# Kernel optimization log

Hardware: AMD Instinct MI355X
Metric: run time of the kernel (lower is better)

## Reference

```python
import jax, jax.numpy as jnp
import numpy as np

BS, NN = 4096, 16          # batch size, robots per sample
OBS_PN, ACT_PN = 10, 2     # per-node obs / action dims
HID = 128                  # hidden_dim; hidden_depth = 2
N = BS * NN                # total nodes


def _build_edges():
    # complete graph per sample including self-loops (PyG GCNConv adds self-loops;
    # self-loop weight exp(-0)=1 matches PyG fill_value=1.0)
    s = np.repeat(np.arange(NN), NN)
    d = np.tile(np.arange(NN), NN)
    off = np.repeat(np.arange(BS) * NN, NN * NN)
    src = np.tile(s, BS) + off
    dst = np.tile(d, BS) + off
    return jnp.asarray(src, jnp.int32), jnp.asarray(dst, jnp.int32)


def setup_inputs() -> dict:
    key = jax.random.key(0)
    ks = jax.random.split(key, 16)
    inp = {
        "obs": jax.random.normal(ks[0], (BS, NN * OBS_PN), jnp.float32),
        "action": jax.random.normal(ks[1], (BS, NN * ACT_PN), jnp.float32),
    }
    dims = [(OBS_PN, HID), (HID, HID), (HID, 1)]  # trunk_input_size = 10
    i = 2
    for q in ("Q1", "Q2"):
        for l, (din, dout) in enumerate(dims):
            inp[f"{q}_W{l}"] = jax.random.normal(ks[i], (din, dout), jnp.float32) / np.sqrt(din).astype(np.float32)
            inp[f"{q}_b{l}"] = jnp.zeros((dout,), jnp.float32)
            i += 1
    inp["src"], inp["dst"] = _build_edges()
    return inp


def _gcn(x, W, b, src, dst, norm):
    # GCNConv: out = scatter_add(norm * (x @ W)[src] -> dst) + b
    y = x @ W                                  # [N, F_out]
    msg = norm[:, None] * y[src]               # [E, F_out]
    return jax.ops.segment_sum(msg, dst, num_segments=N) + b


def reference(obs, action, Q1_W0, Q1_b0, Q1_W1, Q1_b1, Q1_W2, Q1_b2,
              Q2_W0, Q2_b0, Q2_W1, Q2_b1, Q2_W2, Q2_b2, src, dst):
    feat = jnp.concatenate(
        [obs.reshape(N, OBS_PN), action.reshape(N, ACT_PN)], axis=-1)  # [N, 12]
    loc = feat[:, :2]          # robot_loc
    x = feat[:, ACT_PN:]       # input_features[:, gnn_action_dim:] -> [N, 10]

    # per-edge distance weights + symmetric GCN normalization
    w = jnp.exp(-jnp.linalg.norm(loc[dst] - loc[src], axis=-1))        # [E]
    deg = jax.ops.segment_sum(w, dst, num_segments=N)                  # [N]
    dinv = jnp.where(deg > 0, deg, 1.0) ** -0.5
    norm = dinv[src] * w * dinv[dst]

    def net(W0, b0, W1, b1, W2, b2):
        h = jax.nn.relu(_gcn(x, W0, b0, src, dst, norm))
        h = jax.nn.relu(_gcn(h, W1, b1, src, dst, norm))
        return _gcn(h, W2, b2, src, dst, norm).reshape(BS, NN)

    q1 = net(Q1_W0, Q1_b0, Q1_W1, Q1_b1, Q1_W2, Q1_b2)
    q2 = net(Q2_W0, Q2_b0, Q2_W1, Q2_b1, Q2_W2, Q2_b2)
    return (q1, q2)
```

## Files before the change

### kernel.cpp

```cpp
#include <hip/hip_runtime.h>


typedef short    s16x8 __attribute__((ext_vector_type(8)));
typedef float    f32x4 __attribute__((ext_vector_type(4)));
typedef unsigned u32x4 __attribute__((ext_vector_type(4)));

#define MFMA32(a, b, c) __builtin_amdgcn_mfma_f32_16x16x32_bf16((a), (b), (c), 0, 0, 0)

constexpr int WS_W0F = 0;
constexpr int WS_W1  = 8192;

constexpr int LDS_RAW    = 65536;
constexpr int SMEM_TOTAL = 65536 + 8 * 200 * 4;

__device__ __forceinline__ unsigned short bf16_rn(float f) {
  unsigned u = __float_as_uint(f);
  u = u + 0x7FFFu + ((u >> 16) & 1u);
  return (unsigned short)(u >> 16);
}
__device__ __forceinline__ void split2(float f, unsigned short& h, unsigned short& l) {
  h = bf16_rn(f);
  float fh = __uint_as_float(((unsigned)h) << 16);
  l = bf16_rn(f - fh);
}
__device__ __forceinline__ void split_pk(float f0, float f1,
                                         unsigned& H, unsigned& L) {
  unsigned u0 = __float_as_uint(f0) + 0x8000u;
  unsigned u1 = __float_as_uint(f1) + 0x8000u;
  H = __builtin_amdgcn_perm(u1, u0, 0x07060302u);
  float r0 = f0 - __uint_as_float(u0 & 0xFFFF0000u);
  float r1 = f1 - __uint_as_float(u1 & 0xFFFF0000u);
  L = __builtin_amdgcn_perm(__float_as_uint(r1), __float_as_uint(r0), 0x07060302u);
}
__device__ __forceinline__ s16x8 as_s16x8(u32x4 v) {
  return __builtin_bit_cast(s16x8, v);
}

extern "C" __global__ void __launch_bounds__(256)
prep_weights(const float* __restrict__ w0a, const float* __restrict__ w1a,
             const float* __restrict__ w0b, const float* __restrict__ w1b,
             unsigned short* __restrict__ ws) {
  const int tid = threadIdx.x;
  if (blockIdx.x < 16) {
    int f = blockIdx.x * 256 + tid;
    int lane = f & 63, t = (f >> 6) & 7, q = (f >> 9) & 3, net = f >> 11;
    const float* W1 = net ? w1b : w1a;
    int c = 16 * t + (lane & 15);
    int kbase = 32 * q + 4 * (lane >> 4);
    s16x8 v;
#pragma unroll
    for (int e = 0; e < 8; ++e) {
      int k = kbase + (e & 3) + 16 * (e >> 2);
      v[e] = (short)bf16_rn(W1[k * 128 + c]);
    }
    ((s16x8*)(ws + WS_W1))[((net * 4 + q) * 8 + t) * 64 + lane] = v;
  } else {
#pragma unroll
    for (int i = 0; i < 4; ++i) {
      int f = i * 256 + tid;
      int lane = f & 63, t = (f >> 6) & 7, net = (f >> 9) & 1;
      const float* W0 = net ? w0b : w0a;
      int c = 16 * t + (lane & 15);
      int kbase = 4 * (lane >> 4);
      s16x8 v;
#pragma unroll
      for (int j = 0; j < 4; ++j) {
        int k = kbase + j;
        float w = (k < 10) ? W0[k * 128 + c] : 0.f;
        unsigned short h, l; split2(w, h, l);
        v[j] = (short)h; v[4 + j] = (short)l;
      }
      ((s16x8*)(ws + WS_W0F))[(net * 8 + t) * 64 + lane] = v;
    }
  }
}

extern "C" __global__ void __launch_bounds__(512, 4)
gcnn_critic_kernel(const float* __restrict__ obs, const float* __restrict__ act,
                   const float* __restrict__ b0a, const float* __restrict__ b1a,
                   const float* __restrict__ w2a, const float* __restrict__ b2a,
                   const float* __restrict__ b0b, const float* __restrict__ b1b,
                   const float* __restrict__ w2b, const float* __restrict__ b2b,
                   const unsigned short* __restrict__ ws,
                   float* __restrict__ out) {
  extern __shared__ char smem[];
  const int tid  = threadIdx.x;
  const int lane = tid & 63;
  const int wv   = tid >> 6;
  const int l15  = lane & 15;
  const int lg   = lane >> 4;
  const int batch = blockIdx.x * 8 + wv;

  s16x8* lW = (s16x8*)smem;
  float* raw = (float*)(smem + LDS_RAW) + wv * 200;

  {
    const s16x8* gW = (const s16x8*)(ws + WS_W1);
#pragma unroll
    for (int k = 0; k < 8; ++k) lW[tid + k * 512] = gW[tid + k * 512];
  }
#pragma unroll
  for (int i = 0; i < 3; ++i) {
    int j = i * 64 + lane;
    if (j < 192) {
      float v = (j < 160) ? obs[batch * 160 + j] : act[batch * 32 + (j - 160)];
      raw[j] = v;
    }
  }
  __syncthreads();

  float wreg[4];
  float wsum = 0.f;
#pragma unroll
  for (int j = 0; j < 4; ++j) {
    int s = 4 * lg + j;
    float dx = raw[l15 * 10]     - raw[s * 10];
    float dy = raw[l15 * 10 + 1] - raw[s * 10 + 1];
    float w = expf(-sqrtf(dx * dx + dy * dy));
    wreg[j] = w;
    wsum += w;
  }
  wsum += __shfl_xor(wsum, 16, 64);
  wsum += __shfl_xor(wsum, 32, 64);
  float dv = 1.0f / sqrtf(wsum);
  float Af[4];
#pragma unroll
  for (int j = 0; j < 4; ++j) {
    float dvs = __shfl(dv, 4 * lg + j, 64);
    Af[j] = wreg[j] * dv * dvs;
  }
  unsigned AH01, AL01, AH23, AL23;
  split_pk(Af[0], Af[1], AH01, AL01);
  split_pk(Af[2], Af[3], AH23, AL23);
  const s16x8 ABh = as_s16x8((u32x4){AH01, AH23, AH01, AH23});
  const s16x8 ABl = as_s16x8((u32x4){AL01, AL23, 0u, 0u});

  float xv[4];
#pragma unroll
  for (int j = 0; j < 4; ++j) {
    int s = 4 * lg + j;
    float v = 0.f;
    if (l15 < 8)       v = raw[s * 10 + 2 + l15];
    else if (l15 < 10) v = raw[160 + s * 2 + (l15 - 8)];
    xv[j] = v;
  }
  unsigned xH0, xL0, xH1, xL1;
  split_pk(xv[0], xv[1], xH0, xL0);
  split_pk(xv[2], xv[3], xH1, xL1);
  const s16x8 xop = as_s16x8((u32x4){xH0, xH1, xL0, xL1});

  f32x4 z0 = {0.f, 0.f, 0.f, 0.f};
  z0 = MFMA32(xop, ABh, z0);
  z0 = MFMA32(xop, ABl, z0);
  unsigned zH0, zL0, zH1, zL1;
  split_pk(z0[0], z0[1], zH0, zL0);
  split_pk(z0[2], z0[3], zH1, zL1);
  const s16x8 z0op = as_s16x8((u32x4){zH0, zH1, zL0, zL1});

  const s16x8* W0F = (const s16x8*)(ws + WS_W0F);
  const s16x8 zero8 = {0, 0, 0, 0, 0, 0, 0, 0};
  float b2v0 = b2a[0], b2v1 = b2b[0];

#pragma unroll 1
  for (int net = 0; net < 2; ++net) {
    const float* B0 = net ? b0b : b0a;
    const float* B1 = net ? b1b : b1a;
    const float* W2 = net ? w2b : w2a;
    const float b2v = net ? b2v1 : b2v0;

    s16x8 h1op[8];
#pragma unroll
    for (int t = 0; t < 8; ++t) {
      s16x8 wf = W0F[(net * 8 + t) * 64 + lane];
      s16x8 Bh = __builtin_shufflevector(wf, wf, 0, 1, 2, 3, 0, 1, 2, 3);
      s16x8 Bl = __builtin_shufflevector(wf, zero8, 4, 5, 6, 7, 8, 9, 10, 11);
      float bv = B0[16 * t + l15];
      f32x4 a = {0.f, 0.f, 0.f, 0.f};
      a = MFMA32(z0op, Bh, a);
      a = MFMA32(z0op, Bl, a);
      float a0 = fmaxf(a[0] + bv, 0.f), a1 = fmaxf(a[1] + bv, 0.f);
      float a2 = fmaxf(a[2] + bv, 0.f), a3 = fmaxf(a[3] + bv, 0.f);
      unsigned H0, L0, H1, L1;
      split_pk(a0, a1, H0, L0);
      split_pk(a2, a3, H1, L1);
      h1op[t] = as_s16x8((u32x4){H0, H1, L0, L1});
    }

    unsigned zHw[8][2], zLw[8][2];
#pragma unroll
    for (int t = 0; t < 8; ++t) {
      f32x4 z = {0.f, 0.f, 0.f, 0.f};
      z = MFMA32(h1op[t], ABh, z);
      z = MFMA32(h1op[t], ABl, z);
      split_pk(z[0], z[1], zHw[t][0], zLw[t][0]);
      split_pk(z[2], z[3], zHw[t][1], zLw[t][1]);
    }

    f32x4 acc[8];
#pragma unroll
    for (int t = 0; t < 8; ++t) acc[t] = (f32x4){0.f, 0.f, 0.f, 0.f};
    __builtin_amdgcn_s_setprio(1);
#pragma unroll
    for (int q = 0; q < 4; ++q) {
      s16x8 zh8 = as_s16x8(
          (u32x4){zHw[2 * q][0], zHw[2 * q][1], zHw[2 * q + 1][0], zHw[2 * q + 1][1]});
      s16x8 zl8 = as_s16x8(
          (u32x4){zLw[2 * q][0], zLw[2 * q][1], zLw[2 * q + 1][0], zLw[2 * q + 1][1]});
      int base = (net * 4 + q) * 8 * 64 + lane;
#pragma unroll
      for (int t = 0; t < 8; ++t) {
        s16x8 W = lW[base + t * 64];
        acc[t] = MFMA32(zh8, W, acc[t]);
        acc[t] = MFMA32(zl8, W, acc[t]);
      }
    }
    __builtin_amdgcn_s_setprio(0);

    float part[4] = {0.f, 0.f, 0.f, 0.f};
#pragma unroll
    for (int t = 0; t < 8; ++t) {
      float bv  = B1[16 * t + l15];
      float wv2 = W2[16 * t + l15];
#pragma unroll
      for (int r = 0; r < 4; ++r)
        part[r] += fmaxf(acc[t][r] + bv, 0.f) * wv2;
    }
#pragma unroll
    for (int d = 1; d < 16; d <<= 1)
#pragma unroll
      for (int r = 0; r < 4; ++r)
        part[r] += __shfl_xor(part[r], d, 64);
    float pq = Af[0] * part[0] + Af[1] * part[1] + Af[2] * part[2] + Af[3] * part[3];
    pq += __shfl_xor(pq, 16, 64);
    pq += __shfl_xor(pq, 32, 64);
    if (lane < 16)
      out[net * 65536 + batch * 16 + l15] = pq + b2v;
  }
}

extern "C" void kernel_launch(void* const* d_in, const int* in_sizes, int n_in,
                              void* d_out, int out_size, void* d_ws, size_t ws_size,
                              hipStream_t stream) {
  (void)in_sizes; (void)n_in; (void)out_size; (void)ws_size;
  const float* obs = (const float*)d_in[0];
  const float* act = (const float*)d_in[1];
  const float* w0a = (const float*)d_in[2];
  const float* b0a = (const float*)d_in[3];
  const float* w1a = (const float*)d_in[4];
  const float* b1a = (const float*)d_in[5];
  const float* w2a = (const float*)d_in[6];
  const float* b2a = (const float*)d_in[7];
  const float* w0b = (const float*)d_in[8];
  const float* b0b = (const float*)d_in[9];
  const float* w1b = (const float*)d_in[10];
  const float* b1b = (const float*)d_in[11];
  const float* w2b = (const float*)d_in[12];
  const float* b2b = (const float*)d_in[13];
  unsigned short* ws = (unsigned short*)d_ws;

  prep_weights<<<17, 256, 0, stream>>>(w0a, w1a, w0b, w1b, ws);
  gcnn_critic_kernel<<<512, 512, SMEM_TOTAL, stream>>>(
      obs, act, b0a, b1a, w2a, b2a, b0b, b1b, w2b, b2b, ws, (float*)d_out);
}
```

Before: 103.7 us.

## Process two batch samples per wavefront and drop low-half bf16 for layer-2 Z

Each wavefront now handles two samples, and blocks shrink to 256 threads, so each LDS load of a W1 fragment feeds two MFMAs from different samples. The z operand of the 128x128 layer is now packed only as rounded bf16 high halves, with no low-part correction term, which halves the MFMA count in the main loop. This gives up the split-bf16 precision that path had, and the doubled per-wave register state (two accumulator sets) may lower occupancy. The 64 KB LDS copy of W1 is now spread over half as many threads.

```diff
diff --git a/kernel.cpp b/kernel.cpp
--- a/kernel.cpp
+++ b/kernel.cpp
@@ -31,6 +31,10 @@
   float r0 = f0 - __uint_as_float(u0 & 0xFFFF0000u);
   float r1 = f1 - __uint_as_float(u1 & 0xFFFF0000u);
   L = __builtin_amdgcn_perm(__float_as_uint(r1), __float_as_uint(r0), 0x07060302u);
+}
+__device__ __forceinline__ unsigned pack_hi(float f0, float f1) {
+  return __builtin_amdgcn_perm(__float_as_uint(f1) + 0x8000u,
+                               __float_as_uint(f0) + 0x8000u, 0x07060302u);
 }
 __device__ __forceinline__ s16x8 as_s16x8(u32x4 v) {
   return __builtin_bit_cast(s16x8, v);
@@ -75,7 +79,7 @@
   }
 }
 
-extern "C" __global__ void __launch_bounds__(512, 4)
+extern "C" __global__ void __launch_bounds__(256, 2)
 gcnn_critic_kernel(const float* __restrict__ obs, const float* __restrict__ act,
                    const float* __restrict__ b0a, const float* __restrict__ b1a,
                    const float* __restrict__ w2a, const float* __restrict__ b2a,
@@ -89,73 +93,78 @@
   const int wv   = tid >> 6;
   const int l15  = lane & 15;
   const int lg   = lane >> 4;
-  const int batch = blockIdx.x * 8 + wv;
-
-  s16x8* lW = (s16x8*)smem;
-  float* raw = (float*)(smem + LDS_RAW) + wv * 200;
+  const int bb   = blockIdx.x * 8 + wv * 2;
+
+  s16x8* lW  = (s16x8*)smem;
+  float* raw = (float*)(smem + LDS_RAW) + wv * 400;
 
   {
     const s16x8* gW = (const s16x8*)(ws + WS_W1);
 #pragma unroll
-    for (int k = 0; k < 8; ++k) lW[tid + k * 512] = gW[tid + k * 512];
-  }
-#pragma unroll
-  for (int i = 0; i < 3; ++i) {
-    int j = i * 64 + lane;
-    if (j < 192) {
-      float v = (j < 160) ? obs[batch * 160 + j] : act[batch * 32 + (j - 160)];
-      raw[j] = v;
-    }
+    for (int k = 0; k < 16; ++k) lW[tid + k * 256] = gW[tid + k * 256];
+  }
+#pragma unroll
+  for (int i = 0; i < 6; ++i) {
+    int idx = i * 64 + lane;
+    int bi = (idx >= 192) ? 1 : 0;
+    int j = idx - bi * 192;
+    float v = (j < 160) ? obs[(bb + bi) * 160 + j] : act[(bb + bi) * 32 + (j - 160)];
+    raw[bi * 200 + j] = v;
   }
   __syncthreads();
 
-  float wreg[4];
-  float wsum = 0.f;
-#pragma unroll
-  for (int j = 0; j < 4; ++j) {
-    int s = 4 * lg + j;
-    float dx = raw[l15 * 10]     - raw[s * 10];
-    float dy = raw[l15 * 10 + 1] - raw[s * 10 + 1];
-    float w = expf(-sqrtf(dx * dx + dy * dy));
-    wreg[j] = w;
-    wsum += w;
-  }
-  wsum += __shfl_xor(wsum, 16, 64);
-  wsum += __shfl_xor(wsum, 32, 64);
-  float dv = 1.0f / sqrtf(wsum);
-  float Af[4];
-#pragma unroll
-  for (int j = 0; j < 4; ++j) {
-    float dvs = __shfl(dv, 4 * lg + j, 64);
-    Af[j] = wreg[j] * dv * dvs;
-  }
-  unsigned AH01, AL01, AH23, AL23;
-  split_pk(Af[0], Af[1], AH01, AL01);
-  split_pk(Af[2], Af[3], AH23, AL23);
-  const s16x8 ABh = as_s16x8((u32x4){AH01, AH23, AH01, AH23});
-  const s16x8 ABl = as_s16x8((u32x4){AL01, AL23, 0u, 0u});
-
-  float xv[4];
-#pragma unroll
-  for (int j = 0; j < 4; ++j) {
-    int s = 4 * lg + j;
-    float v = 0.f;
-    if (l15 < 8)       v = raw[s * 10 + 2 + l15];
-    else if (l15 < 10) v = raw[160 + s * 2 + (l15 - 8)];
-    xv[j] = v;
-  }
-  unsigned xH0, xL0, xH1, xL1;
-  split_pk(xv[0], xv[1], xH0, xL0);
-  split_pk(xv[2], xv[3], xH1, xL1);
-  const s16x8 xop = as_s16x8((u32x4){xH0, xH1, xL0, xL1});
-
-  f32x4 z0 = {0.f, 0.f, 0.f, 0.f};
-  z0 = MFMA32(xop, ABh, z0);
-  z0 = MFMA32(xop, ABl, z0);
-  unsigned zH0, zL0, zH1, zL1;
-  split_pk(z0[0], z0[1], zH0, zL0);
-  split_pk(z0[2], z0[3], zH1, zL1);
-  const s16x8 z0op = as_s16x8((u32x4){zH0, zH1, zL0, zL1});
+  float Af[2][4];
+  s16x8 ABh[2], ABl[2], z0op[2];
+#pragma unroll
+  for (int bi = 0; bi < 2; ++bi) {
+    const float* rb = raw + bi * 200;
+    float wreg[4];
+    float wsum = 0.f;
+#pragma unroll
+    for (int j = 0; j < 4; ++j) {
+      int s = 4 * lg + j;
+      float dx = rb[l15 * 10]     - rb[s * 10];
+      float dy = rb[l15 * 10 + 1] - rb[s * 10 + 1];
+      float w = expf(-sqrtf(dx * dx + dy * dy));
+      wreg[j] = w;
+      wsum += w;
+    }
+    wsum += __shfl_xor(wsum, 16, 64);
+    wsum += __shfl_xor(wsum, 32, 64);
+    float dv = 1.0f / sqrtf(wsum);
+#pragma unroll
+    for (int j = 0; j < 4; ++j) {
+      float dvs = __shfl(dv, 4 * lg + j, 64);
+      Af[bi][j] = wreg[j] * dv * dvs;
+    }
+    unsigned AH01, AL01, AH23, AL23;
+    split_pk(Af[bi][0], Af[bi][1], AH01, AL01);
+    split_pk(Af[bi][2], Af[bi][3], AH23, AL23);
+    ABh[bi] = as_s16x8((u32x4){AH01, AH23, AH01, AH23});
+    ABl[bi] = as_s16x8((u32x4){AL01, AL23, 0u, 0u});
+
+    float xv[4];
+#pragma unroll
+    for (int j = 0; j < 4; ++j) {
+      int s = 4 * lg + j;
+      float v = 0.f;
+      if (l15 < 8)       v = rb[s * 10 + 2 + l15];
+      else if (l15 < 10) v = rb[160 + s * 2 + (l15 - 8)];
+      xv[j] = v;
+    }
+    unsigned xH0, xL0, xH1, xL1;
+    split_pk(xv[0], xv[1], xH0, xL0);
+    split_pk(xv[2], xv[3], xH1, xL1);
+    s16x8 xop = as_s16x8((u32x4){xH0, xH1, xL0, xL1});
+
+    f32x4 z0 = {0.f, 0.f, 0.f, 0.f};
+    z0 = MFMA32(xop, ABh[bi], z0);
+    z0 = MFMA32(xop, ABl[bi], z0);
+    unsigned zH0, zL0, zH1, zL1;
+    split_pk(z0[0], z0[1], zH0, zL0);
+    split_pk(z0[2], z0[3], zH1, zL1);
+    z0op[bi] = as_s16x8((u32x4){zH0, zH1, zL0, zL1});
+  }
 
   const s16x8* W0F = (const s16x8*)(ws + WS_W0F);
   const s16x8 zero8 = {0, 0, 0, 0, 0, 0, 0, 0};
@@ -168,73 +177,88 @@
     const float* W2 = net ? w2b : w2a;
     const float b2v = net ? b2v1 : b2v0;
 
-    s16x8 h1op[8];
+    s16x8 h1op[2][8];
 #pragma unroll
     for (int t = 0; t < 8; ++t) {
       s16x8 wf = W0F[(net * 8 + t) * 64 + lane];
       s16x8 Bh = __builtin_shufflevector(wf, wf, 0, 1, 2, 3, 0, 1, 2, 3);
       s16x8 Bl = __builtin_shufflevector(wf, zero8, 4, 5, 6, 7, 8, 9, 10, 11);
       float bv = B0[16 * t + l15];
-      f32x4 a = {0.f, 0.f, 0.f, 0.f};
-      a = MFMA32(z0op, Bh, a);
-      a = MFMA32(z0op, Bl, a);
-      float a0 = fmaxf(a[0] + bv, 0.f), a1 = fmaxf(a[1] + bv, 0.f);
-      float a2 = fmaxf(a[2] + bv, 0.f), a3 = fmaxf(a[3] + bv, 0.f);
-      unsigned H0, L0, H1, L1;
-      split_pk(a0, a1, H0, L0);
-      split_pk(a2, a3, H1, L1);
-      h1op[t] = as_s16x8((u32x4){H0, H1, L0, L1});
-    }
-
-    unsigned zHw[8][2], zLw[8][2];
-#pragma unroll
-    for (int t = 0; t < 8; ++t) {
-      f32x4 z = {0.f, 0.f, 0.f, 0.f};
-      z = MFMA32(h1op[t], ABh, z);
-      z = MFMA32(h1op[t], ABl, z);
-      split_pk(z[0], z[1], zHw[t][0], zLw[t][0]);
-      split_pk(z[2], z[3], zHw[t][1], zLw[t][1]);
-    }
-
-    f32x4 acc[8];
-#pragma unroll
-    for (int t = 0; t < 8; ++t) acc[t] = (f32x4){0.f, 0.f, 0.f, 0.f};
+#pragma unroll
+      for (int bi = 0; bi < 2; ++bi) {
+        f32x4 a = {0.f, 0.f, 0.f, 0.f};
+        a = MFMA32(z0op[bi], Bh, a);
+        a = MFMA32(z0op[bi], Bl, a);
+        float a0 = fmaxf(a[0] + bv, 0.f), a1 = fmaxf(a[1] + bv, 0.f);
+        float a2 = fmaxf(a[2] + bv, 0.f), a3 = fmaxf(a[3] + bv, 0.f);
+        unsigned H0, L0, H1, L1;
+        split_pk(a0, a1, H0, L0);
+        split_pk(a2, a3, H1, L1);
+        h1op[bi][t] = as_s16x8((u32x4){H0, H1, L0, L1});
+      }
+    }
+
+    unsigned zHw[2][8][2];
+#pragma unroll
+    for (int t = 0; t < 8; ++t)
+#pragma unroll
+      for (int bi = 0; bi < 2; ++bi) {
+        f32x4 z = {0.f, 0.f, 0.f, 0.f};
+        z = MFMA32(h1op[bi][t], ABh[bi], z);
+        z = MFMA32(h1op[bi][t], ABl[bi], z);
+        zHw[bi][t][0] = pack_hi(z[0], z[1]);
+        zHw[bi][t][1] = pack_hi(z[2], z[3]);
+      }
+
+    f32x4 acc[2][8];
+#pragma unroll
+    for (int bi = 0; bi < 2; ++bi)
+#pragma unroll
+      for (int t = 0; t < 8; ++t) acc[bi][t] = (f32x4){0.f, 0.f, 0.f, 0.f};
     __builtin_amdgcn_s_setprio(1);
 #pragma unroll
     for (int q = 0; q < 4; ++q) {
-      s16x8 zh8 = as_s16x8(
-          (u32x4){zHw[2 * q][0], zHw[2 * q][1], zHw[2 * q + 1][0], zHw[2 * q + 1][1]});
-      s16x8 zl8 = as_s16x8(
-          (u32x4){zLw[2 * q][0], zLw[2 * q][1], zLw[2 * q + 1][0], zLw[2 * q + 1][1]});
+      s16x8 zA = as_s16x8((u32x4){zHw[0][2 * q][0], zHw[0][2 * q][1],
+                                  zHw[0][2 * q + 1][0], zHw[0][2 * q + 1][1]});
+      s16x8 zB = as_s16x8((u32x4){zHw[1][2 * q][0], zHw[1][2 * q][1],
+                                  zHw[1][2 * q + 1][0], zHw[1][2 * q + 1][1]});
       int base = (net * 4 + q) * 8 * 64 + lane;
 #pragma unroll
       for (int t = 0; t < 8; ++t) {
         s16x8 W = lW[base + t * 64];
-        acc[t] = MFMA32(zh8, W, acc[t]);
-        acc[t] = MFMA32(zl8, W, acc[t]);
+        acc[0][t] = MFMA32(zA, W, acc[0][t]);
+        acc[1][t] = MFMA32(zB, W, acc[1][t]);
       }
     }
     __builtin_amdgcn_s_setprio(0);
 
-    float part[4] = {0.f, 0.f, 0.f, 0.f};
+    float part[2][4] = {{0.f, 0.f, 0.f, 0.f}, {0.f, 0.f, 0.f, 0.f}};
 #pragma unroll
     for (int t = 0; t < 8; ++t) {
       float bv  = B1[16 * t + l15];
       float wv2 = W2[16 * t + l15];
 #pragma unroll
-      for (int r = 0; r < 4; ++r)
-        part[r] += fmaxf(acc[t][r] + bv, 0.f) * wv2;
+      for (int bi = 0; bi < 2; ++bi)
+#pragma unroll
+        for (int r = 0; r < 4; ++r)
+          part[bi][r] += fmaxf(acc[bi][t][r] + bv, 0.f) * wv2;
     }
 #pragma unroll
     for (int d = 1; d < 16; d <<= 1)
 #pragma unroll
-      for (int r = 0; r < 4; ++r)
-        part[r] += __shfl_xor(part[r], d, 64);
-    float pq = Af[0] * part[0] + Af[1] * part[1] + Af[2] * part[2] + Af[3] * part[3];
-    pq += __shfl_xor(pq, 16, 64);
-    pq += __shfl_xor(pq, 32, 64);
-    if (lane < 16)
-      out[net * 65536 + batch * 16 + l15] = pq + b2v;
+      for (int bi = 0; bi < 2; ++bi)
+#pragma unroll
+        for (int r = 0; r < 4; ++r)
+          part[bi][r] += __shfl_xor(part[bi][r], d, 64);
+#pragma unroll
+    for (int bi = 0; bi < 2; ++bi) {
+      float pq = Af[bi][0] * part[bi][0] + Af[bi][1] * part[bi][1] +
+                 Af[bi][2] * part[bi][2] + Af[bi][3] * part[bi][3];
+      pq += __shfl_xor(pq, 16, 64);
+      pq += __shfl_xor(pq, 32, 64);
+      if (lane < 16)
+        out[net * 65536 + (bb + bi) * 16 + l15] = pq + b2v;
+    }
   }
 }
 
@@ -259,6 +283,6 @@
   unsigned short* ws = (unsigned short*)d_ws;
 
   prep_weights<<<17, 256, 0, stream>>>(w0a, w1a, w0b, w1b, ws);
-  gcnn_critic_kernel<<<512, 512, SMEM_TOTAL, stream>>>(
+  gcnn_critic_kernel<<<512, 256, SMEM_TOTAL, stream>>>(
       obs, act, b0a, b1a, w2a, b2a, b0b, b1b, w2b, b2b, ws, (float*)d_out);
 }
```

Result: no change. 104.9 us (+1.1%).
